# Performance work log

Measured on AMD Instinct MI355X. Metric: run time of the kernel, lower is better.

## Reference

```python
import jax, jax.numpy as jnp
import numpy as np

VOCAB, EMBED, HIDDEN = 256, 512, 1024
B, T = 64, 512


def setup_inputs() -> dict:
    key = jax.random.key(0)
    ks = jax.random.split(key, 12)
    s = 0.02
    return {
        "x": jax.random.randint(ks[0], (B, T), 0, VOCAB),
        "embed": jax.random.normal(ks[1], (VOCAB, EMBED), jnp.float32) * s,
        "Wih0": jax.random.normal(ks[2], (3 * HIDDEN, EMBED), jnp.float32) * s,
        "Whh0": jax.random.normal(ks[3], (3 * HIDDEN, HIDDEN), jnp.float32) * s,
        "bih0": jax.random.normal(ks[4], (3 * HIDDEN,), jnp.float32) * s,
        "bhh0": jax.random.normal(ks[5], (3 * HIDDEN,), jnp.float32) * s,
        "Wih1": jax.random.normal(ks[6], (3 * HIDDEN, HIDDEN), jnp.float32) * s,
        "Whh1": jax.random.normal(ks[7], (3 * HIDDEN, HIDDEN), jnp.float32) * s,
        "bih1": jax.random.normal(ks[8], (3 * HIDDEN,), jnp.float32) * s,
        "bhh1": jax.random.normal(ks[9], (3 * HIDDEN,), jnp.float32) * s,
        "W_out": jax.random.normal(ks[10], (VOCAB, HIDDEN), jnp.float32) * s,
        "b_out": jax.random.normal(ks[11], (VOCAB,), jnp.float32) * s,
    }


def gru_cell(inp, h, Wih, Whh, bih, bhh):
    # PyTorch GRUCell math.
    gi = inp @ Wih.T + bih  # (B, 3H)
    gh = h @ Whh.T + bhh    # (B, 3H)
    i_r, i_z, i_n = jnp.split(gi, 3, axis=-1)
    h_r, h_z, h_n = jnp.split(gh, 3, axis=-1)
    r = jax.nn.sigmoid(i_r + h_r)
    z = jax.nn.sigmoid(i_z + h_z)
    n = jnp.tanh(i_n + r * h_n)
    return (1.0 - z) * n + z * h


def reference(x, embed, Wih0, Whh0, bih0, bhh0, Wih1, Whh1, bih1, bhh1, W_out, b_out):
    emb = embed[x]                       # (B, T, E)
    xs = jnp.swapaxes(emb, 0, 1)         # (T, B, E)
    h0 = jnp.zeros((x.shape[0], HIDDEN), emb.dtype)

    def step(carry, inp_t):
        h_0, h_1 = carry
        h_0 = gru_cell(inp_t, h_0, Wih0, Whh0, bih0, bhh0)
        h_1 = gru_cell(h_0, h_1, Wih1, Whh1, bih1, bhh1)
        return (h_0, h_1), h_1

    _, outs = jax.lax.scan(step, (h0, h0), xs)   # outs: (T, B, H)
    outs = jnp.swapaxes(outs, 0, 1)              # (B, T, H)
    logits = outs @ W_out.T + b_out              # (B, T, V)
    return logits
```

## Files before the change

kernel.cpp:

```cpp
#include <hip/hip_runtime.h>
#include <stdint.h>

typedef short short8 __attribute__((ext_vector_type(8)));
typedef float f32x4 __attribute__((ext_vector_type(4)));
typedef unsigned short u16;

#define MFMA16(a, b, c) __builtin_amdgcn_mfma_f32_16x16x32_bf16((a), (b), (c), 0, 0, 0)

#define T_LEN 512
#define BATCH 64
#define EMB_D 512
#define HID 1024
#define VOC 256
#define NWG 128
#define RNN_THREADS 512
#define R0 256
#define R1 8
#define SLOT (BATCH * HID)

#define OFF_XT    0u
#define OFF_EMBT  131072u
#define OFF_WIH0  524288u
#define OFF_WHH0  3670016u
#define OFF_WIH1  9961472u
#define OFF_WHH1  16252928u
#define OFF_WOUT  22544384u
#define OFF_H0R   23068672u
#define OFF_H1R   56623104u
#define OFF_H1ALL 57671680u
#define OFF_SYNC  124780544u
#define SYNC_BYTES 16640u
#define WS_TOTAL  (OFF_SYNC + SYNC_BYTES)

static __device__ __forceinline__ u16 f2b(float f) {
  uint32_t u = __float_as_uint(f);
  u += 0x7FFFu + ((u >> 16) & 1u);
  return (u16)(u >> 16);
}
static __device__ __forceinline__ float sigm(float x) { return 1.0f / (1.0f + __expf(-x)); }

__global__ void cvt_kernel(const float* __restrict__ src, u16* __restrict__ dst, int n) {
  int i = ((int)blockIdx.x * 256 + (int)threadIdx.x) * 4;
  if (i + 4 <= n) {
    const float4 v = *(const float4*)(src + i);
    ushort4 o;
    o.x = f2b(v.x); o.y = f2b(v.y); o.z = f2b(v.z); o.w = f2b(v.w);
    *(ushort4*)(dst + i) = o;
  }
}

__global__ void xt_kernel(const int* __restrict__ x, int* __restrict__ xT) {
  const int t = (int)blockIdx.x, b = (int)threadIdx.x;
  xT[t * BATCH + b] = x[b * T_LEN + t];
}

static __device__ __forceinline__ void poll_flags(unsigned* p0, unsigned* p1,
                                                  unsigned t0, unsigned t1, int tid) {
  if (tid < 128) {
    unsigned* f = (tid < 64) ? (p0 + (size_t)tid * 32) : (p1 + (size_t)(tid - 64) * 32);
    const unsigned tgt = (tid < 64) ? t0 : t1;
    while (__hip_atomic_load(f, __ATOMIC_RELAXED, __HIP_MEMORY_SCOPE_AGENT) < tgt)
      __builtin_amdgcn_s_sleep(1);
  }
  __syncthreads();
}

__global__ __launch_bounds__(RNN_THREADS, 1) void rnn_persist_kernel(
    const int* __restrict__ xT, const u16* __restrict__ embtab,
    const u16* __restrict__ A0i_r, const u16* __restrict__ A0i_z, const u16* __restrict__ A0i_n,
    const u16* __restrict__ A0h_r, const u16* __restrict__ A0h_z, const u16* __restrict__ A0h_n,
    const u16* __restrict__ A1i_r, const u16* __restrict__ A1i_z, const u16* __restrict__ A1i_n,
    const u16* __restrict__ A1h_r, const u16* __restrict__ A1h_z, const u16* __restrict__ A1h_n,
    const float* __restrict__ bih0, const float* __restrict__ bhh0,
    const float* __restrict__ bih1, const float* __restrict__ bhh1,
    u16* __restrict__ h0r, u16* __restrict__ h1r,
    u16* __restrict__ h1all, unsigned* __restrict__ sync)
{
  __shared__ __align__(16) float lds[16384];
  const int tid = (int)threadIdx.x;
  const int wv = tid >> 6;
  const int lane = tid & 63;
  const int lrow = lane & 15;
  const int lk8 = (lane >> 4) << 3;
  const int wgid = (int)blockIdx.x;
  const int layer = wgid >> 6;
  const int ubase = (wgid & 63) << 4;
  const bool iwave = (wv < 4);
  const bool l0i = (layer == 0) && iwave;
  unsigned* p0 = sync;
  unsigned* p1 = sync + 64 * 32;

  const u16 *Ar, *Az, *An;
  int ldb, k0;
  if (layer == 0) {
    if (iwave) { Ar = A0i_r; Az = A0i_z; An = A0i_n; ldb = EMB_D; k0 = wv * 128; }
    else       { Ar = A0h_r; Az = A0h_z; An = A0h_n; ldb = HID;   k0 = (wv - 4) * 256; }
  } else {
    if (iwave) { Ar = A1i_r; Az = A1i_z; An = A1i_n; ldb = HID;   k0 = wv * 256; }
    else       { Ar = A1h_r; Az = A1h_z; An = A1h_n; ldb = HID;   k0 = (wv - 4) * 256; }
  }
  const size_t arow = (size_t)(ubase + lrow) * ldb;

  const float* bi = layer ? bih1 : bih0;
  const float* bh = layer ? bhh1 : bhh0;
  const int u0 = (tid & 7) * 2;
  const int eb = tid >> 3;
  const int eug0 = ubase + u0, eug1 = eug0 + 1;
  const float bR0 = bi[eug0] + bh[eug0];
  const float bZ0 = bi[HID + eug0] + bh[HID + eug0];
  const float bNi0 = bi[2 * HID + eug0];
  const float bNh0 = bh[2 * HID + eug0];
  const float bR1 = bi[eug1] + bh[eug1];
  const float bZ1 = bi[HID + eug1] + bh[HID + eug1];
  const float bNi1 = bi[2 * HID + eug1];
  const float bNh1 = bh[2 * HID + eug1];
  const int l_e = ((u0 >> 2) << 4) | (eb & 15);
  const int r0 = u0 & 3, r1 = r0 + 1;
  const int ebt = eb >> 4;
  const int ix0 = l_e ^ (r0 << 3), ix1 = l_e ^ (r1 << 3);
  float hp0 = 0.f, hp1 = 0.f;

  const int sBeg = (layer == 0) ? 0 : 1;
  const int sEnd = (layer == 0) ? (T_LEN - 1) : T_LEN;

  for (int s = sBeg; s <= sEnd; ++s) {
    if (layer == 0) {
      const unsigned bp = (s >= 252) ? (unsigned)(s - 250) : 0u;
      poll_flags(p0, p1, (unsigned)s, bp, tid);
    } else {
      poll_flags(p0, p1, (unsigned)s, (unsigned)(s - 1), tid);
    }

    {
      const u16* h0prev = h0r + (size_t)((s - 1) & (R0 - 1)) * SLOT;
      const u16* h1prev = h1r + (size_t)((s - 2) & (R1 - 1)) * SLOT;

      f32x4 acc0[4], acc1[4], accn[4];
#pragma unroll
      for (int bt = 0; bt < 4; ++bt) {
        acc0[bt] = (f32x4){0.f, 0.f, 0.f, 0.f};
        acc1[bt] = (f32x4){0.f, 0.f, 0.f, 0.f};
        accn[bt] = (f32x4){0.f, 0.f, 0.f, 0.f};
      }
      if (l0i) {
        const u16* brow[4];
#pragma unroll
        for (int bt = 0; bt < 4; ++bt) {
          const int tok = xT[s * BATCH + bt * 16 + lrow];
          brow[bt] = embtab + (size_t)tok * EMB_D;
        }
#pragma unroll
        for (int ks = 0; ks < 4; ++ks) {
          const int kk = k0 + ks * 32 + lk8;
          const short8 ar = *(const short8*)(Ar + arow + kk);
          const short8 az = *(const short8*)(Az + arow + kk);
          const short8 an = *(const short8*)(An + arow + kk);
          const short8 b0 = *(const short8*)(brow[0] + kk);
          const short8 b1 = *(const short8*)(brow[1] + kk);
          const short8 b2 = *(const short8*)(brow[2] + kk);
          const short8 b3 = *(const short8*)(brow[3] + kk);
          acc0[0] = MFMA16(ar, b0, acc0[0]); acc1[0] = MFMA16(az, b0, acc1[0]); accn[0] = MFMA16(an, b0, accn[0]);
          acc0[1] = MFMA16(ar, b1, acc0[1]); acc1[1] = MFMA16(az, b1, acc1[1]); accn[1] = MFMA16(an, b1, accn[1]);
          acc0[2] = MFMA16(ar, b2, acc0[2]); acc1[2] = MFMA16(az, b2, acc1[2]); accn[2] = MFMA16(an, b2, accn[2]);
          acc0[3] = MFMA16(ar, b3, acc0[3]); acc1[3] = MFMA16(az, b3, acc1[3]); accn[3] = MFMA16(an, b3, accn[3]);
        }
      } else {
        const u16* Bp;
        if (layer == 0) Bp = h0prev;
        else            Bp = iwave ? h0prev : h1prev;
#pragma unroll
        for (int ks = 0; ks < 8; ++ks) {
          const int kk = k0 + ks * 32 + lk8;
          const short8 ar = *(const short8*)(Ar + arow + kk);
          const short8 az = *(const short8*)(Az + arow + kk);
          const short8 an = *(const short8*)(An + arow + kk);
#pragma unroll
          for (int bt = 0; bt < 4; ++bt) {
            const short8 bf = *(const short8*)(Bp + (size_t)(bt * 16 + lrow) * HID + kk);
            acc0[bt] = MFMA16(ar, bf, acc0[bt]);
            acc1[bt] = MFMA16(az, bf, acc1[bt]);
            accn[bt] = MFMA16(an, bf, accn[bt]);
          }
        }
      }
      if (iwave) {
#pragma unroll
        for (int bt = 0; bt < 4; ++bt)
#pragma unroll
          for (int r = 0; r < 4; ++r) {
            const int ix = lane ^ (r << 3);
            lds[(((wv * 4 + 0) * 4 + bt) * 256) + r * 64 + ix] = acc0[bt][r];
            lds[(((wv * 4 + 1) * 4 + bt) * 256) + r * 64 + ix] = acc1[bt][r];
            lds[(((wv * 4 + 2) * 4 + bt) * 256) + r * 64 + ix] = accn[bt][r];
          }
      }
      __syncthreads();
      if (!iwave) {
        const int z = wv - 4;
#pragma unroll
        for (int bt = 0; bt < 4; ++bt)
#pragma unroll
          for (int r = 0; r < 4; ++r) {
            const int ix = lane ^ (r << 3);
            float* q0 = &lds[(((z * 4 + 0) * 4 + bt) * 256) + r * 64 + ix];
            float* q1 = &lds[(((z * 4 + 1) * 4 + bt) * 256) + r * 64 + ix];
            *q0 = *q0 + acc0[bt][r];
            *q1 = *q1 + acc1[bt][r];
            lds[(((z * 4 + 3) * 4 + bt) * 256) + r * 64 + ix] = accn[bt][r];
          }
      }
      __syncthreads();
      {
        float sr0 = 0.f, sz0 = 0.f, sni0 = 0.f, snh0 = 0.f;
        float sr1 = 0.f, sz1 = 0.f, sni1 = 0.f, snh1 = 0.f;
#pragma unroll
        for (int z = 0; z < 4; ++z) {
          sr0  += lds[(((z * 4 + 0) * 4 + ebt) * 256) + r0 * 64 + ix0];
          sz0  += lds[(((z * 4 + 1) * 4 + ebt) * 256) + r0 * 64 + ix0];
          sni0 += lds[(((z * 4 + 2) * 4 + ebt) * 256) + r0 * 64 + ix0];
          snh0 += lds[(((z * 4 + 3) * 4 + ebt) * 256) + r0 * 64 + ix0];
          sr1  += lds[(((z * 4 + 0) * 4 + ebt) * 256) + r1 * 64 + ix1];
          sz1  += lds[(((z * 4 + 1) * 4 + ebt) * 256) + r1 * 64 + ix1];
          sni1 += lds[(((z * 4 + 2) * 4 + ebt) * 256) + r1 * 64 + ix1];
          snh1 += lds[(((z * 4 + 3) * 4 + ebt) * 256) + r1 * 64 + ix1];
        }
        const float rg0 = sigm(sr0 + bR0);
        const float zg0 = sigm(sz0 + bZ0);
        const float ng0 = tanhf(sni0 + bNi0 + rg0 * (snh0 + bNh0));
        const float hn0 = (1.0f - zg0) * ng0 + zg0 * hp0;
        const float rg1 = sigm(sr1 + bR1);
        const float zg1 = sigm(sz1 + bZ1);
        const float ng1 = tanhf(sni1 + bNi1 + rg1 * (snh1 + bNh1));
        const float hn1 = (1.0f - zg1) * ng1 + zg1 * hp1;
        hp0 = hn0; hp1 = hn1;
        const unsigned packed = (unsigned)f2b(hn0) | ((unsigned)f2b(hn1) << 16);
        u16* wslot = layer ? (h1r + (size_t)((s - 1) & (R1 - 1)) * SLOT)
                           : (h0r + (size_t)(s & (R0 - 1)) * SLOT);
        __hip_atomic_store((unsigned*)&wslot[eb * HID + eug0], packed,
                           __ATOMIC_RELAXED, __HIP_MEMORY_SCOPE_AGENT);
        if (layer)
          *(unsigned*)&h1all[((size_t)(s - 1) * BATCH + eb) * HID + eug0] = packed;
      }
    }
    __syncthreads();
    if (tid == 0) {
      unsigned* f = layer ? (p1 + (size_t)(wgid - 64) * 32) : (p0 + (size_t)wgid * 32);
      __hip_atomic_store(f, (unsigned)(s + (layer ? 0 : 1)), __ATOMIC_RELAXED,
                         __HIP_MEMORY_SCOPE_AGENT);
    }
  }
}

__global__ __launch_bounds__(256, 2) void logits_kernel(
    const u16* __restrict__ h1all, const u16* __restrict__ Woutb,
    const float* __restrict__ bout, float* __restrict__ out)
{
  __shared__ __align__(16) short lds[16 * 4 * 64 * 8];
  const int tid = (int)threadIdx.x;
  const int wv = tid >> 6, lane = tid & 63;
  const int lrow = lane & 15, lk8 = (lane >> 4) << 3;
  const int row0 = (int)blockIdx.x * 64 + wv * 16;
  f32x4 acc[16];
#pragma unroll
  for (int i = 0; i < 16; ++i) acc[i] = (f32x4){0.f, 0.f, 0.f, 0.f};

  for (int kc = 0; kc < HID; kc += 128) {
    __syncthreads();
#pragma unroll
    for (int j = 0; j < 16; ++j) {
      const int slot = tid + j * 256;
      const int ct = slot >> 8, kt = (slot >> 6) & 3, l = slot & 63;
      *(short8*)&lds[slot * 8] =
          *(const short8*)(Woutb + (size_t)(ct * 16 + (l & 15)) * HID + kc + kt * 32 + ((l >> 4) << 3));
    }
    __syncthreads();
#pragma unroll
    for (int kt = 0; kt < 4; ++kt) {
      const short8 af = *(const short8*)(h1all + (size_t)(row0 + lrow) * HID + kc + kt * 32 + lk8);
#pragma unroll
      for (int ct = 0; ct < 16; ++ct) {
        const short8 bf = *(const short8*)&lds[((ct * 4 + kt) * 64 + lane) * 8];
        acc[ct] = MFMA16(af, bf, acc[ct]);
      }
    }
  }
#pragma unroll
  for (int ct = 0; ct < 16; ++ct) {
    const int v = ct * 16 + lrow;
    const float bo = bout[v];
#pragma unroll
    for (int r = 0; r < 4; ++r) {
      const int row = row0 + (lane >> 4) * 4 + r;
      const int t = row >> 6, b = row & 63;
      out[((size_t)(b * T_LEN + t)) * VOC + v] = acc[ct][r] + bo;
    }
  }
}

extern "C" void kernel_launch(void* const* d_in, const int* in_sizes, int n_in,
                              void* d_out, int out_size, void* d_ws, size_t ws_size,
                              hipStream_t stream) {
  const int*   x     = (const int*)d_in[0];
  const float* embed = (const float*)d_in[1];
  const float* Wih0  = (const float*)d_in[2];
  const float* Whh0  = (const float*)d_in[3];
  const float* bih0  = (const float*)d_in[4];
  const float* bhh0  = (const float*)d_in[5];
  const float* Wih1  = (const float*)d_in[6];
  const float* Whh1  = (const float*)d_in[7];
  const float* bih1  = (const float*)d_in[8];
  const float* bhh1  = (const float*)d_in[9];
  const float* Wout  = (const float*)d_in[10];
  const float* bout  = (const float*)d_in[11];
  float* out = (float*)d_out;
  char* ws = (char*)d_ws;
  if (ws_size < (size_t)WS_TOTAL) return;

  hipMemsetAsync(ws + OFF_H0R + (size_t)(R0 - 1) * SLOT * 2, 0, SLOT * 2, stream);
  hipMemsetAsync(ws + OFF_H1R + (size_t)(R1 - 1) * SLOT * 2, 0, SLOT * 2, stream);
  hipMemsetAsync(ws + OFF_SYNC, 0, SYNC_BYTES, stream);
  xt_kernel<<<512, 64, 0, stream>>>(x, (int*)(ws + OFF_XT));
  cvt_kernel<<<128, 256, 0, stream>>>(embed, (u16*)(ws + OFF_EMBT), 256 * 512);
  cvt_kernel<<<1536, 256, 0, stream>>>(Wih0, (u16*)(ws + OFF_WIH0), 3072 * 512);
  cvt_kernel<<<3072, 256, 0, stream>>>(Whh0, (u16*)(ws + OFF_WHH0), 3072 * 1024);
  cvt_kernel<<<3072, 256, 0, stream>>>(Wih1, (u16*)(ws + OFF_WIH1), 3072 * 1024);
  cvt_kernel<<<3072, 256, 0, stream>>>(Whh1, (u16*)(ws + OFF_WHH1), 3072 * 1024);
  cvt_kernel<<<256, 256, 0, stream>>>(Wout, (u16*)(ws + OFF_WOUT), 256 * 1024);

  const u16* wih0b = (const u16*)(ws + OFF_WIH0);
  const u16* whh0b = (const u16*)(ws + OFF_WHH0);
  const u16* wih1b = (const u16*)(ws + OFF_WIH1);
  const u16* whh1b = (const u16*)(ws + OFF_WHH1);

  rnn_persist_kernel<<<NWG, RNN_THREADS, 0, stream>>>(
      (const int*)(ws + OFF_XT), (const u16*)(ws + OFF_EMBT),
      wih0b, wih0b + 524288, wih0b + 1048576,
      whh0b, whh0b + 1048576, whh0b + 2097152,
      wih1b, wih1b + 1048576, wih1b + 2097152,
      whh1b, whh1b + 1048576, whh1b + 2097152,
      bih0, bhh0, bih1, bhh1,
      (u16*)(ws + OFF_H0R), (u16*)(ws + OFF_H1R),
      (u16*)(ws + OFF_H1ALL), (unsigned*)(ws + OFF_SYNC));

  logits_kernel<<<512, 256, 0, stream>>>((const u16*)(ws + OFF_H1ALL),
                                         (const u16*)(ws + OFF_WOUT), bout, out);
}
```

Baseline: 7.787 ms.

## Repartition persistent GRU across batch groups with per-wave flags, dropping LDS reduction

The persistent RNN kernel now runs 256 blocks of two waves each, split as 4 batch groups × 2 layers × 32 unit groups. Each wave computes the full K reduction for 16 units and 16 batch rows, so the cross-wave LDS reduction and the block barriers go away. Synchronisation moves to per-wave flags within each batch group, and every lane polls one flag with no __syncthreads. In exchange each block redoes the long serial K loop alone with fewer MFMA chains in flight per wave. Weight reads also repeat across the four batch groups.

```diff
diff --git a/kernel.cpp b/kernel.cpp
--- a/kernel.cpp
+++ b/kernel.cpp
@@ -4,6 +4,7 @@
 typedef short short8 __attribute__((ext_vector_type(8)));
 typedef float f32x4 __attribute__((ext_vector_type(4)));
 typedef unsigned short u16;
+typedef unsigned long long u64;
 
 #define MFMA16(a, b, c) __builtin_amdgcn_mfma_f32_16x16x32_bf16((a), (b), (c), 0, 0, 0)
 
@@ -12,8 +13,8 @@
 #define EMB_D 512
 #define HID 1024
 #define VOC 256
-#define NWG 128
-#define RNN_THREADS 512
+#define NWG 256
+#define THREADS 128
 #define R0 256
 #define R1 8
 #define SLOT (BATCH * HID)
@@ -29,7 +30,7 @@
 #define OFF_H1R   56623104u
 #define OFF_H1ALL 57671680u
 #define OFF_SYNC  124780544u
-#define SYNC_BYTES 16640u
+#define SYNC_BYTES 65536u
 #define WS_TOTAL  (OFF_SYNC + SYNC_BYTES)
 
 static __device__ __forceinline__ u16 f2b(float f) {
@@ -54,18 +55,7 @@
   xT[t * BATCH + b] = x[b * T_LEN + t];
 }
 
-static __device__ __forceinline__ void poll_flags(unsigned* p0, unsigned* p1,
-                                                  unsigned t0, unsigned t1, int tid) {
-  if (tid < 128) {
-    unsigned* f = (tid < 64) ? (p0 + (size_t)tid * 32) : (p1 + (size_t)(tid - 64) * 32);
-    const unsigned tgt = (tid < 64) ? t0 : t1;
-    while (__hip_atomic_load(f, __ATOMIC_RELAXED, __HIP_MEMORY_SCOPE_AGENT) < tgt)
-      __builtin_amdgcn_s_sleep(1);
-  }
-  __syncthreads();
-}
-
-__global__ __launch_bounds__(RNN_THREADS, 1) void rnn_persist_kernel(
+__global__ __launch_bounds__(THREADS, 1) void rnn_persist_kernel(
     const int* __restrict__ xT, const u16* __restrict__ embtab,
     const u16* __restrict__ A0i_r, const u16* __restrict__ A0i_z, const u16* __restrict__ A0i_n,
     const u16* __restrict__ A0h_r, const u16* __restrict__ A0h_z, const u16* __restrict__ A0h_n,
@@ -76,178 +66,143 @@
     u16* __restrict__ h0r, u16* __restrict__ h1r,
     u16* __restrict__ h1all, unsigned* __restrict__ sync)
 {
-  __shared__ __align__(16) float lds[16384];
   const int tid = (int)threadIdx.x;
   const int wv = tid >> 6;
   const int lane = tid & 63;
   const int lrow = lane & 15;
   const int lk8 = (lane >> 4) << 3;
-  const int wgid = (int)blockIdx.x;
-  const int layer = wgid >> 6;
-  const int ubase = (wgid & 63) << 4;
-  const bool iwave = (wv < 4);
-  const bool l0i = (layer == 0) && iwave;
+  const int bb = (int)blockIdx.x >> 6;
+  const int g = (int)blockIdx.x & 63;
+  const int layer = g >> 5;
+  const int ub = g & 31;
+
   unsigned* p0 = sync;
-  unsigned* p1 = sync + 64 * 32;
-
-  const u16 *Ar, *Az, *An;
-  int ldb, k0;
-  if (layer == 0) {
-    if (iwave) { Ar = A0i_r; Az = A0i_z; An = A0i_n; ldb = EMB_D; k0 = wv * 128; }
-    else       { Ar = A0h_r; Az = A0h_z; An = A0h_n; ldb = HID;   k0 = (wv - 4) * 256; }
-  } else {
-    if (iwave) { Ar = A1i_r; Az = A1i_z; An = A1i_n; ldb = HID;   k0 = wv * 256; }
-    else       { Ar = A1h_r; Az = A1h_z; An = A1h_n; ldb = HID;   k0 = (wv - 4) * 256; }
-  }
-  const size_t arow = (size_t)(ubase + lrow) * ldb;
+  unsigned* p1 = sync + 4 * 64 * 32;
+  const int widx = ub * 2 + wv;
+  unsigned* myflag = (layer ? p1 : p0) + (size_t)(bb * 64 + widx) * 32;
+  unsigned* pollf0 = p0 + (size_t)(bb * 64 + lane) * 32;
+  unsigned* pollf1 = p1 + (size_t)(bb * 64 + lane) * 32;
+
+  const u16 *Axr, *Axz, *Axn, *Ahr, *Ahz, *Ahn;
+  int ldx;
+  if (layer == 0) { Axr = A0i_r; Axz = A0i_z; Axn = A0i_n;
+                    Ahr = A0h_r; Ahz = A0h_z; Ahn = A0h_n; ldx = EMB_D; }
+  else            { Axr = A1i_r; Axz = A1i_z; Axn = A1i_n;
+                    Ahr = A1h_r; Ahz = A1h_z; Ahn = A1h_n; ldx = HID; }
+  const int urow = ub * 32 + wv * 16 + lrow;
+  const size_t axrow = (size_t)urow * ldx;
+  const size_t ahrow = (size_t)urow * HID;
+  const int brow = bb * 16 + lrow;
 
   const float* bi = layer ? bih1 : bih0;
   const float* bh = layer ? bhh1 : bhh0;
-  const int u0 = (tid & 7) * 2;
-  const int eb = tid >> 3;
-  const int eug0 = ubase + u0, eug1 = eug0 + 1;
-  const float bR0 = bi[eug0] + bh[eug0];
-  const float bZ0 = bi[HID + eug0] + bh[HID + eug0];
-  const float bNi0 = bi[2 * HID + eug0];
-  const float bNh0 = bh[2 * HID + eug0];
-  const float bR1 = bi[eug1] + bh[eug1];
-  const float bZ1 = bi[HID + eug1] + bh[HID + eug1];
-  const float bNi1 = bi[2 * HID + eug1];
-  const float bNh1 = bh[2 * HID + eug1];
-  const int l_e = ((u0 >> 2) << 4) | (eb & 15);
-  const int r0 = u0 & 3, r1 = r0 + 1;
-  const int ebt = eb >> 4;
-  const int ix0 = l_e ^ (r0 << 3), ix1 = l_e ^ (r1 << 3);
-  float hp0 = 0.f, hp1 = 0.f;
-
-  const int sBeg = (layer == 0) ? 0 : 1;
-  const int sEnd = (layer == 0) ? (T_LEN - 1) : T_LEN;
+  const int ubase_l = ub * 32 + wv * 16 + (lane >> 4) * 4;
+  const int batch = bb * 16 + (lane & 15);
+  float bR[4], bZ[4], bNi[4], bNh[4], hp[4];
+#pragma unroll
+  for (int r = 0; r < 4; ++r) {
+    const int ug = ubase_l + r;
+    bR[r] = bi[ug] + bh[ug];
+    bZ[r] = bi[HID + ug] + bh[HID + ug];
+    bNi[r] = bi[2 * HID + ug];
+    bNh[r] = bh[2 * HID + ug];
+    hp[r] = 0.f;
+  }
+  const size_t hoff = (size_t)batch * HID + ubase_l;
+
+  const int sBeg = layer ? 1 : 0;
+  const int sEnd = layer ? T_LEN : (T_LEN - 1);
 
   for (int s = sBeg; s <= sEnd; ++s) {
+    {
+      const unsigned t0 = (unsigned)s;
+      unsigned v = __hip_atomic_load(pollf0, __ATOMIC_RELAXED, __HIP_MEMORY_SCOPE_AGENT);
+      while (v < t0) { __builtin_amdgcn_s_sleep(1);
+        v = __hip_atomic_load(pollf0, __ATOMIC_RELAXED, __HIP_MEMORY_SCOPE_AGENT); }
+    }
+    if (layer) {
+      const unsigned t1 = (unsigned)(s - 1);
+      unsigned v = __hip_atomic_load(pollf1, __ATOMIC_RELAXED, __HIP_MEMORY_SCOPE_AGENT);
+      while (v < t1) { __builtin_amdgcn_s_sleep(1);
+        v = __hip_atomic_load(pollf1, __ATOMIC_RELAXED, __HIP_MEMORY_SCOPE_AGENT); }
+    } else if (s >= 252) {
+      const unsigned t1 = (unsigned)(s - 250);
+      unsigned v = __hip_atomic_load(pollf1, __ATOMIC_RELAXED, __HIP_MEMORY_SCOPE_AGENT);
+      while (v < t1) { __builtin_amdgcn_s_sleep(1);
+        v = __hip_atomic_load(pollf1, __ATOMIC_RELAXED, __HIP_MEMORY_SCOPE_AGENT); }
+    }
+
+    const u16* h0p = h0r + (size_t)((s - 1) & (R0 - 1)) * SLOT;
+    const u16* h1p = h1r + (size_t)((s - 2) & (R1 - 1)) * SLOT;
+
+    f32x4 aR = {0.f, 0.f, 0.f, 0.f}, aZ = aR, aNi = aR, aNh = aR;
+
     if (layer == 0) {
-      const unsigned bp = (s >= 252) ? (unsigned)(s - 250) : 0u;
-      poll_flags(p0, p1, (unsigned)s, bp, tid);
+      const int tok = xT[s * BATCH + brow];
+      const u16* Bx = embtab + (size_t)tok * EMB_D;
+#pragma unroll 8
+      for (int ks = 0; ks < 16; ++ks) {
+        const int kk = ks * 32 + lk8;
+        const short8 ar = *(const short8*)(Axr + axrow + kk);
+        const short8 az = *(const short8*)(Axz + axrow + kk);
+        const short8 an = *(const short8*)(Axn + axrow + kk);
+        const short8 bf = *(const short8*)(Bx + kk);
+        aR = MFMA16(ar, bf, aR);
+        aZ = MFMA16(az, bf, aZ);
+        aNi = MFMA16(an, bf, aNi);
+      }
     } else {
-      poll_flags(p0, p1, (unsigned)s, (unsigned)(s - 1), tid);
-    }
-
+      const u16* Bx = h0p + (size_t)brow * HID;
+#pragma unroll 8
+      for (int ks = 0; ks < 32; ++ks) {
+        const int kk = ks * 32 + lk8;
+        const short8 ar = *(const short8*)(Axr + axrow + kk);
+        const short8 az = *(const short8*)(Axz + axrow + kk);
+        const short8 an = *(const short8*)(Axn + axrow + kk);
+        const short8 bf = *(const short8*)(Bx + kk);
+        aR = MFMA16(ar, bf, aR);
+        aZ = MFMA16(az, bf, aZ);
+        aNi = MFMA16(an, bf, aNi);
+      }
+    }
     {
-      const u16* h0prev = h0r + (size_t)((s - 1) & (R0 - 1)) * SLOT;
-      const u16* h1prev = h1r + (size_t)((s - 2) & (R1 - 1)) * SLOT;
-
-      f32x4 acc0[4], acc1[4], accn[4];
-#pragma unroll
-      for (int bt = 0; bt < 4; ++bt) {
-        acc0[bt] = (f32x4){0.f, 0.f, 0.f, 0.f};
-        acc1[bt] = (f32x4){0.f, 0.f, 0.f, 0.f};
-        accn[bt] = (f32x4){0.f, 0.f, 0.f, 0.f};
+      const u16* Bh = (layer ? h1p : h0p) + (size_t)brow * HID;
+#pragma unroll 8
+      for (int ks = 0; ks < 32; ++ks) {
+        const int kk = ks * 32 + lk8;
+        const short8 ar = *(const short8*)(Ahr + ahrow + kk);
+        const short8 az = *(const short8*)(Ahz + ahrow + kk);
+        const short8 an = *(const short8*)(Ahn + ahrow + kk);
+        const short8 bf = *(const short8*)(Bh + kk);
+        aR = MFMA16(ar, bf, aR);
+        aZ = MFMA16(az, bf, aZ);
+        aNh = MFMA16(an, bf, aNh);
       }
-      if (l0i) {
-        const u16* brow[4];
-#pragma unroll
-        for (int bt = 0; bt < 4; ++bt) {
-          const int tok = xT[s * BATCH + bt * 16 + lrow];
-          brow[bt] = embtab + (size_t)tok * EMB_D;
-        }
-#pragma unroll
-        for (int ks = 0; ks < 4; ++ks) {
-          const int kk = k0 + ks * 32 + lk8;
-          const short8 ar = *(const short8*)(Ar + arow + kk);
-          const short8 az = *(const short8*)(Az + arow + kk);
-          const short8 an = *(const short8*)(An + arow + kk);
-          const short8 b0 = *(const short8*)(brow[0] + kk);
-          const short8 b1 = *(const short8*)(brow[1] + kk);
-          const short8 b2 = *(const short8*)(brow[2] + kk);
-          const short8 b3 = *(const short8*)(brow[3] + kk);
-          acc0[0] = MFMA16(ar, b0, acc0[0]); acc1[0] = MFMA16(az, b0, acc1[0]); accn[0] = MFMA16(an, b0, accn[0]);
-          acc0[1] = MFMA16(ar, b1, acc0[1]); acc1[1] = MFMA16(az, b1, acc1[1]); accn[1] = MFMA16(an, b1, accn[1]);
-          acc0[2] = MFMA16(ar, b2, acc0[2]); acc1[2] = MFMA16(az, b2, acc1[2]); accn[2] = MFMA16(an, b2, accn[2]);
-          acc0[3] = MFMA16(ar, b3, acc0[3]); acc1[3] = MFMA16(az, b3, acc1[3]); accn[3] = MFMA16(an, b3, accn[3]);
-        }
-      } else {
-        const u16* Bp;
-        if (layer == 0) Bp = h0prev;
-        else            Bp = iwave ? h0prev : h1prev;
-#pragma unroll
-        for (int ks = 0; ks < 8; ++ks) {
-          const int kk = k0 + ks * 32 + lk8;
-          const short8 ar = *(const short8*)(Ar + arow + kk);
-          const short8 az = *(const short8*)(Az + arow + kk);
-          const short8 an = *(const short8*)(An + arow + kk);
-#pragma unroll
-          for (int bt = 0; bt < 4; ++bt) {
-            const short8 bf = *(const short8*)(Bp + (size_t)(bt * 16 + lrow) * HID + kk);
-            acc0[bt] = MFMA16(ar, bf, acc0[bt]);
-            acc1[bt] = MFMA16(az, bf, acc1[bt]);
-            accn[bt] = MFMA16(an, bf, accn[bt]);
-          }
-        }
-      }
-      if (iwave) {
-#pragma unroll
-        for (int bt = 0; bt < 4; ++bt)
-#pragma unroll
-          for (int r = 0; r < 4; ++r) {
-            const int ix = lane ^ (r << 3);
-            lds[(((wv * 4 + 0) * 4 + bt) * 256) + r * 64 + ix] = acc0[bt][r];
-            lds[(((wv * 4 + 1) * 4 + bt) * 256) + r * 64 + ix] = acc1[bt][r];
-            lds[(((wv * 4 + 2) * 4 + bt) * 256) + r * 64 + ix] = accn[bt][r];
-          }
-      }
-      __syncthreads();
-      if (!iwave) {
-        const int z = wv - 4;
-#pragma unroll
-        for (int bt = 0; bt < 4; ++bt)
-#pragma unroll
-          for (int r = 0; r < 4; ++r) {
-            const int ix = lane ^ (r << 3);
-            float* q0 = &lds[(((z * 4 + 0) * 4 + bt) * 256) + r * 64 + ix];
-            float* q1 = &lds[(((z * 4 + 1) * 4 + bt) * 256) + r * 64 + ix];
-            *q0 = *q0 + acc0[bt][r];
-            *q1 = *q1 + acc1[bt][r];
-            lds[(((z * 4 + 3) * 4 + bt) * 256) + r * 64 + ix] = accn[bt][r];
-          }
-      }
-      __syncthreads();
-      {
-        float sr0 = 0.f, sz0 = 0.f, sni0 = 0.f, snh0 = 0.f;
-        float sr1 = 0.f, sz1 = 0.f, sni1 = 0.f, snh1 = 0.f;
-#pragma unroll
-        for (int z = 0; z < 4; ++z) {
-          sr0  += lds[(((z * 4 + 0) * 4 + ebt) * 256) + r0 * 64 + ix0];
-          sz0  += lds[(((z * 4 + 1) * 4 + ebt) * 256) + r0 * 64 + ix0];
-          sni0 += lds[(((z * 4 + 2) * 4 + ebt) * 256) + r0 * 64 + ix0];
-          snh0 += lds[(((z * 4 + 3) * 4 + ebt) * 256) + r0 * 64 + ix0];
-          sr1  += lds[(((z * 4 + 0) * 4 + ebt) * 256) + r1 * 64 + ix1];
-          sz1  += lds[(((z * 4 + 1) * 4 + ebt) * 256) + r1 * 64 + ix1];
-          sni1 += lds[(((z * 4 + 2) * 4 + ebt) * 256) + r1 * 64 + ix1];
-          snh1 += lds[(((z * 4 + 3) * 4 + ebt) * 256) + r1 * 64 + ix1];
-        }
-        const float rg0 = sigm(sr0 + bR0);
-        const float zg0 = sigm(sz0 + bZ0);
-        const float ng0 = tanhf(sni0 + bNi0 + rg0 * (snh0 + bNh0));
-        const float hn0 = (1.0f - zg0) * ng0 + zg0 * hp0;
-        const float rg1 = sigm(sr1 + bR1);
-        const float zg1 = sigm(sz1 + bZ1);
-        const float ng1 = tanhf(sni1 + bNi1 + rg1 * (snh1 + bNh1));
-        const float hn1 = (1.0f - zg1) * ng1 + zg1 * hp1;
-        hp0 = hn0; hp1 = hn1;
-        const unsigned packed = (unsigned)f2b(hn0) | ((unsigned)f2b(hn1) << 16);
-        u16* wslot = layer ? (h1r + (size_t)((s - 1) & (R1 - 1)) * SLOT)
-                           : (h0r + (size_t)(s & (R0 - 1)) * SLOT);
-        __hip_atomic_store((unsigned*)&wslot[eb * HID + eug0], packed,
-                           __ATOMIC_RELAXED, __HIP_MEMORY_SCOPE_AGENT);
-        if (layer)
-          *(unsigned*)&h1all[((size_t)(s - 1) * BATCH + eb) * HID + eug0] = packed;
-      }
-    }
-    __syncthreads();
-    if (tid == 0) {
-      unsigned* f = layer ? (p1 + (size_t)(wgid - 64) * 32) : (p0 + (size_t)wgid * 32);
-      __hip_atomic_store(f, (unsigned)(s + (layer ? 0 : 1)), __ATOMIC_RELAXED,
-                         __HIP_MEMORY_SCOPE_AGENT);
-    }
+    }
+    u16 hv0, hv1, hv2, hv3;
+#pragma unroll
+    for (int r = 0; r < 4; ++r) {
+      const float rg = sigm(aR[r] + bR[r]);
+      const float zg = sigm(aZ[r] + bZ[r]);
+      const float ng = tanhf(aNi[r] + bNi[r] + rg * (aNh[r] + bNh[r]));
+      const float hn = (1.0f - zg) * ng + zg * hp[r];
+      hp[r] = hn;
+      const u16 hv = f2b(hn);
+      if (r == 0) hv0 = hv; else if (r == 1) hv1 = hv;
+      else if (r == 2) hv2 = hv; else hv3 = hv;
+    }
+    const u64 packed = (u64)hv0 | ((u64)hv1 << 16) | ((u64)hv2 << 32) | ((u64)hv3 << 48);
+    u16* wslot = layer ? (h1r + (size_t)((s - 1) & (R1 - 1)) * SLOT)
+                       : (h0r + (size_t)(s & (R0 - 1)) * SLOT);
+    __hip_atomic_store((u64*)(wslot + hoff), packed,
+                       __ATOMIC_RELAXED, __HIP_MEMORY_SCOPE_AGENT);
+    if (layer)
+      *(u64*)(h1all + ((size_t)(s - 1) * BATCH + batch) * HID + ubase_l) = packed;
+
+    asm volatile("s_waitcnt vmcnt(0)" ::: "memory");
+    if (lane == 0)
+      __hip_atomic_store(myflag, (unsigned)(layer ? s : s + 1),
+                         __ATOMIC_RELAXED, __HIP_MEMORY_SCOPE_AGENT);
   }
 }
 
@@ -332,7 +287,7 @@
   const u16* wih1b = (const u16*)(ws + OFF_WIH1);
   const u16* whh1b = (const u16*)(ws + OFF_WHH1);
 
-  rnn_persist_kernel<<<NWG, RNN_THREADS, 0, stream>>>(
+  rnn_persist_kernel<<<NWG, THREADS, 0, stream>>>(
       (const int*)(ws + OFF_XT), (const u16*)(ws + OFF_EMBT),
       wih0b, wih0b + 524288, wih0b + 1048576,
       whh0b, whh0b + 1048576, whh0b + 2097152,
```

Result: slower. 9.401 ms (+20.7%).
